# Kernel tuning notes

Hardware: AMD Instinct MI355X
Metric: run time of the kernel (lower is better)

## Reference

```python
import jax, jax.numpy as jnp
import numpy as np

B, E, N, D, L = 16, 1024, 2048, 256, 3


def setup_inputs() -> dict:
    key = jax.random.key(0)
    ks = jax.random.split(key, 8)
    return {
        "evidences_mat": jax.random.normal(ks[0], (B, E, D), jnp.float32),
        "entities_mat": jax.random.normal(ks[1], (B, N, D), jnp.float32),
        "ev_to_ent": jax.random.bernoulli(ks[2], 0.05, (B, E, N)).astype(jnp.float32),
        "ent_to_ev": jax.random.bernoulli(ks[3], 0.05, (B, N, E)).astype(jnp.float32),
        "w_weight": jax.random.normal(ks[4], (L, D, D), jnp.float32) * 0.05,
        "w_bias": jax.random.normal(ks[5], (L, D), jnp.float32) * 0.05,
        "watt_weight": jax.random.normal(ks[6], (L, D, D), jnp.float32) * 0.05,
        "watt_bias": jax.random.normal(ks[7], (L, D), jnp.float32) * 0.05,
    }


def reference(evidences_mat, entities_mat, ev_to_ent, ent_to_ev,
              w_weight, w_bias, watt_weight, watt_bias):
    ev, ent = evidences_mat, entities_mat
    for i in range(L):
        # attention projections (torch Linear: x @ W.T + b)
        pe = jnp.einsum('bed,od->beo', ev, watt_weight[i]) + watt_bias[i]   # [B,E,D]
        pn = jnp.einsum('bnd,od->bno', ent, watt_weight[i]) + watt_bias[i]  # [B,N,D]
        # evidences -> entities messages
        ev_att = jnp.einsum('bed,bnd->ben', pe, pn) * ev_to_ent             # [B,E,N]
        ev_att = jax.nn.softmax(ev_att, axis=1)                              # over E (dim=1)
        msg_ent = jnp.einsum('ben,bed->bnd', ev_att, ev)                     # [B,N,D]
        msg_ent = jnp.einsum('bnd,od->bno', msg_ent, w_weight[i]) + w_bias[i]
        self_ent = jnp.einsum('bnd,od->bno', ent, w_weight[i]) + w_bias[i]
        ent = jax.nn.relu(msg_ent + self_ent)
        # entities -> evidences messages (uses UPDATED entities, as in source)
        ent_att = jnp.einsum('bnd,bed->bne', pn, pe) * ent_to_ev            # [B,N,E]
        ent_att = jax.nn.softmax(ent_att, axis=1)                            # over N (dim=1)
        msg_ev = jnp.einsum('bne,bnd->bed', ent_att, ent)                    # [B,E,D]
        msg_ev = jnp.einsum('bed,od->beo', msg_ev, w_weight[i]) + w_bias[i]
        self_ev = jnp.einsum('bed,od->beo', ev, w_weight[i]) + w_bias[i]
        ev = jax.nn.relu(msg_ev + self_ev)
        # dropout is a no-op (p=0.0 / eval)
    return ent, ev
```

## Files before the change

kernel.cpp:

```cpp
#include <hip/hip_runtime.h>

#define BB 16
#define EE 1024
#define NN 2048
#define DD 256
#define LL 3

typedef _Float16 half8 __attribute__((ext_vector_type(8)));
typedef _Float16 half4 __attribute__((ext_vector_type(4)));
typedef _Float16 half2_t __attribute__((ext_vector_type(2)));
typedef float f32x4 __attribute__((ext_vector_type(4)));

__device__ __forceinline__ void pmerge(float& m, float& s, float m2, float s2) {
    float nm = fmaxf(m, m2);
    s = s * __expf(m - nm) + s2 * __expf(m2 - nm);
    m = nm;
}

__device__ __forceinline__ unsigned pk2(_Float16 a, _Float16 b) {
    union { _Float16 h[2]; unsigned u; } x;
    x.h[0] = a; x.h[1] = b;
    return x.u;
}

__global__ void split_cast(const float* __restrict__ in, _Float16* __restrict__ hi,
                           _Float16* __restrict__ lo, size_t n) {
    size_t stride = (size_t)gridDim.x * blockDim.x * 4;
    for (size_t i = ((size_t)blockIdx.x * blockDim.x + threadIdx.x) * 4; i < n; i += stride) {
        float4 v = *(const float4*)&in[i];
        half4 hh, ll;
        _Float16 h;
        h = (_Float16)v.x; hh[0] = h; ll[0] = (_Float16)(v.x - (float)h);
        h = (_Float16)v.y; hh[1] = h; ll[1] = (_Float16)(v.y - (float)h);
        h = (_Float16)v.z; hh[2] = h; ll[2] = (_Float16)(v.z - (float)h);
        h = (_Float16)v.w; hh[3] = h; ll[3] = (_Float16)(v.w - (float)h);
        *(half4*)&hi[i] = hh;
        *(half4*)&lo[i] = ll;
    }
}

__global__ void cast_u8(const float* __restrict__ in, unsigned char* __restrict__ out, size_t n) {
    size_t stride = (size_t)gridDim.x * blockDim.x * 4;
    for (size_t i = ((size_t)blockIdx.x * blockDim.x + threadIdx.x) * 4; i < n; i += stride) {
        float4 v = *(const float4*)&in[i];
        unsigned int pack = (unsigned int)(unsigned char)v.x |
                            ((unsigned int)(unsigned char)v.y << 8) |
                            ((unsigned int)(unsigned char)v.z << 16) |
                            ((unsigned int)(unsigned char)v.w << 24);
        *(unsigned int*)&out[i] = pack;
    }
}

__global__ void transpose_split(const float* __restrict__ in, _Float16* __restrict__ oh,
                                _Float16* __restrict__ olo, int R, int C) {
    int b = blockIdx.z;
    int c0 = blockIdx.x * 64, r0 = blockIdx.y * 64;
    const float* ib = in + (size_t)b * R * C;
    size_t ob = (size_t)b * R * C;
    __shared__ float tile[64][65];
    int t = threadIdx.x;
    int cl = t & 63, rb = t >> 6;
#pragma unroll
    for (int j = 0; j < 16; j++) {
        int rl = rb + j * 4;
        tile[rl][cl] = ib[(size_t)(r0 + rl) * C + c0 + cl];
    }
    __syncthreads();
    int oc = t >> 2, q = t & 3;
    half8 h0, h1, l0, l1;
#pragma unroll
    for (int i = 0; i < 8; i++) {
        float v = tile[q * 16 + i][oc];
        _Float16 h = (_Float16)v;
        h0[i] = h; l0[i] = (_Float16)(v - (float)h);
    }
#pragma unroll
    for (int i = 0; i < 8; i++) {
        float v = tile[q * 16 + 8 + i][oc];
        _Float16 h = (_Float16)v;
        h1[i] = h; l1[i] = (_Float16)(v - (float)h);
    }
    size_t o = ob + (size_t)(c0 + oc) * R + r0 + q * 16;
    *(half8*)&oh[o] = h0; *(half8*)&oh[o + 8] = h1;
    *(half8*)&olo[o] = l0; *(half8*)&olo[o + 8] = l1;
}

__global__ void transpose_split_perm(const float* __restrict__ in, _Float16* __restrict__ oh,
                                     _Float16* __restrict__ olo, int R, int C) {
    int b = blockIdx.z;
    int c0 = blockIdx.x * 64, r0 = blockIdx.y * 64;
    const float* ib = in + (size_t)b * R * C;
    size_t ob = (size_t)b * R * C;
    __shared__ float tile[64][65];
    int t = threadIdx.x;
    int cl = t & 63, rb = t >> 6;
#pragma unroll
    for (int j = 0; j < 16; j++) {
        int rl = rb + j * 4;
        tile[rl][cl] = ib[(size_t)(r0 + rl) * C + c0 + cl];
    }
    __syncthreads();
    int oc = t >> 2, q = t & 3;
    int g = q >> 1, sub = q & 1;
#pragma unroll
    for (int j = 0; j < 8; j++) {
        int x = sub * 8 + j;
        float v1 = tile[g * 32 + x][oc];
        float v2 = tile[g * 32 + x + 16][oc];
        _Float16 a = (_Float16)v1, b2 = (_Float16)v2;
        _Float16 la = (_Float16)(v1 - (float)a), lb = (_Float16)(v2 - (float)b2);
        size_t o = ob + (size_t)(c0 + oc) * R + r0 + g * 32 + 2 * x;
        half2_t hp; hp[0] = a; hp[1] = b2;
        half2_t lp; lp[0] = la; lp[1] = lb;
        *(half2_t*)&oh[o] = hp;
        *(half2_t*)&olo[o] = lp;
    }
}

__global__ void transpose_u8(const float* __restrict__ in, unsigned char* __restrict__ out,
                             int R, int C) {
    int b = blockIdx.z;
    int c0 = blockIdx.x * 64, r0 = blockIdx.y * 64;
    const float* ib = in + (size_t)b * R * C;
    unsigned char* ob = out + (size_t)b * R * C;
    __shared__ float tile[64][65];
    int t = threadIdx.x;
    int cl = t & 63, rb = t >> 6;
#pragma unroll
    for (int j = 0; j < 16; j++) {
        int rl = rb + j * 4;
        tile[rl][cl] = ib[(size_t)(r0 + rl) * C + c0 + cl];
    }
    __syncthreads();
    int oc = t >> 2, q = t & 3;
    union { unsigned char b[16]; uint4 v; } u;
#pragma unroll
    for (int i = 0; i < 16; i++) u.b[i] = (unsigned char)tile[q * 16 + i][oc];
    size_t o = (size_t)(c0 + oc) * R + r0 + q * 16;
    *(uint4*)&ob[o] = u.v;
}

template <bool A_SPLIT, bool B_SPLIT, bool HAS_BIAS, bool RELU, bool HAS_ADD,
          bool WRITE_F32, bool WRITE_SPLIT, bool B_BATCHED>
__global__ __launch_bounds__(256) void gemm_nt(
    const _Float16* __restrict__ Ah, const _Float16* __restrict__ Al,
    const _Float16* __restrict__ Bh, const _Float16* __restrict__ Bl,
    const float* __restrict__ bias, float bscale,
    const float* __restrict__ addsrc,
    float* __restrict__ Cf, _Float16* __restrict__ Chi, _Float16* __restrict__ Clo,
    int M, int Nn, int K) {
    const int bz = blockIdx.z;
    const int m0 = blockIdx.x * 128, n0 = blockIdx.y * 128;
    const int t = threadIdx.x, lane = t & 63, wid = t >> 6;
    const int wm = wid >> 1, wn = wid & 1;
    const size_t offA = (size_t)bz * M * K;
    const size_t offB = B_BATCHED ? (size_t)bz * Nn * K : (size_t)0;
    const _Float16* Abh = Ah + offA;
    const _Float16* Abl = A_SPLIT ? (Al + offA) : nullptr;
    const _Float16* Bbh = Bh + offB;
    const _Float16* Bbl = B_SPLIT ? (Bl + offB) : nullptr;

    __shared__ _Float16 sAh[128 * 32];
    __shared__ _Float16 sBh[128 * 32];
    __shared__ _Float16 sAl[A_SPLIT ? 128 * 32 : 1];
    __shared__ _Float16 sBl[B_SPLIT ? 128 * 32 : 1];

    f32x4 acc[4][4] = {};
    const int nk = K >> 5;

    auto gA = [&](const _Float16* base, int kt, int q) {
        return *(const uint4*)(base + (size_t)(m0 + (q >> 2)) * K + (kt << 5) + ((q & 3) << 3));
    };
    auto gB = [&](const _Float16* base, int kt, int q) {
        return *(const uint4*)(base + (size_t)(n0 + (q >> 2)) * K + (kt << 5) + ((q & 3) << 3));
    };

    uint4 rah0 = gA(Abh, 0, t), rah1 = gA(Abh, 0, t + 256);
    uint4 rbh0 = gB(Bbh, 0, t), rbh1 = gB(Bbh, 0, t + 256);
    uint4 ral0 = {}, ral1 = {}, rbl0 = {}, rbl1 = {};
    if (A_SPLIT) { ral0 = gA(Abl, 0, t); ral1 = gA(Abl, 0, t + 256); }
    if (B_SPLIT) { rbl0 = gB(Bbl, 0, t); rbl1 = gB(Bbl, 0, t + 256); }

    for (int kt = 0; kt < nk; ++kt) {
        __syncthreads();
        ((uint4*)sAh)[t] = rah0; ((uint4*)sAh)[t + 256] = rah1;
        ((uint4*)sBh)[t] = rbh0; ((uint4*)sBh)[t + 256] = rbh1;
        if (A_SPLIT) { ((uint4*)sAl)[t] = ral0; ((uint4*)sAl)[t + 256] = ral1; }
        if (B_SPLIT) { ((uint4*)sBl)[t] = rbl0; ((uint4*)sBl)[t + 256] = rbl1; }
        __syncthreads();
        if (kt + 1 < nk) {
            rah0 = gA(Abh, kt + 1, t); rah1 = gA(Abh, kt + 1, t + 256);
            rbh0 = gB(Bbh, kt + 1, t); rbh1 = gB(Bbh, kt + 1, t + 256);
            if (A_SPLIT) { ral0 = gA(Abl, kt + 1, t); ral1 = gA(Abl, kt + 1, t + 256); }
            if (B_SPLIT) { rbl0 = gB(Bbl, kt + 1, t); rbl1 = gB(Bbl, kt + 1, t + 256); }
        }
        half8 afh[4], bfh[4], afl[4], bfl[4];
#pragma unroll
        for (int mi = 0; mi < 4; mi++) {
            int off = (wm * 64 + mi * 16 + (lane & 15)) * 32 + ((lane >> 4) << 3);
            afh[mi] = *(const half8*)&sAh[off];
            if (A_SPLIT) afl[mi] = *(const half8*)&sAl[off];
        }
#pragma unroll
        for (int nj = 0; nj < 4; nj++) {
            int off = (wn * 64 + nj * 16 + (lane & 15)) * 32 + ((lane >> 4) << 3);
            bfh[nj] = *(const half8*)&sBh[off];
            if (B_SPLIT) bfl[nj] = *(const half8*)&sBl[off];
        }
#pragma unroll
        for (int mi = 0; mi < 4; mi++)
#pragma unroll
            for (int nj = 0; nj < 4; nj++) {
                acc[mi][nj] = __builtin_amdgcn_mfma_f32_16x16x32_f16(afh[mi], bfh[nj], acc[mi][nj], 0, 0, 0);
                if (B_SPLIT)
                    acc[mi][nj] = __builtin_amdgcn_mfma_f32_16x16x32_f16(afh[mi], bfl[nj], acc[mi][nj], 0, 0, 0);
                if (A_SPLIT)
                    acc[mi][nj] = __builtin_amdgcn_mfma_f32_16x16x32_f16(afl[mi], bfh[nj], acc[mi][nj], 0, 0, 0);
            }
    }

    const int rbase = (lane >> 4) * 4, cc = lane & 15;
#pragma unroll
    for (int mi = 0; mi < 4; mi++) {
#pragma unroll
        for (int nj = 0; nj < 4; nj++) {
            int gn = n0 + wn * 64 + nj * 16 + cc;
            float bv = HAS_BIAS ? bias[gn] * bscale : 0.f;
#pragma unroll
            for (int r = 0; r < 4; r++) {
                int gm = m0 + wm * 64 + mi * 16 + rbase + r;
                float v = acc[mi][nj][r];
                if (HAS_BIAS) v += bv;
                size_t off = ((size_t)bz * M + gm) * Nn + gn;
                if (HAS_ADD) v += addsrc[off];
                if (RELU) v = fmaxf(v, 0.f);
                if (WRITE_F32) Cf[off] = v;
                if (WRITE_SPLIT) {
                    _Float16 h = (_Float16)v;
                    Chi[off] = h;
                    Clo[off] = (_Float16)(v - (float)h);
                }
            }
        }
    }
}

template <bool TRANSA>
__global__ __launch_bounds__(256) void fused_agg(
    const float* __restrict__ S_, const unsigned char* __restrict__ Mk,
    const float2* __restrict__ st, const _Float16* __restrict__ Bh,
    const _Float16* __restrict__ Bl, const float* __restrict__ addsrc,
    _Float16* __restrict__ Xhi, _Float16* __restrict__ Xlo,
    int M, int K) {
    const int bz = blockIdx.z;
    const int m0 = blockIdx.x * 64, n0 = blockIdx.y * 128;
    const int t = threadIdx.x, lane = t & 63, wid = t >> 6;
    const int wm = wid >> 1, wn = wid & 1;
    const float* Sb = S_ + (size_t)bz * EE * NN;
    const unsigned char* Mb = Mk + (size_t)bz * EE * NN;
    const float2* stb = st + (size_t)bz * M;
    const _Float16* Bbh = Bh + (size_t)bz * DD * K;
    const _Float16* Bbl = Bl + (size_t)bz * DD * K;

    __shared__ _Float16 sA[64 * 32];
    __shared__ _Float16 sBh[128 * 32];
    __shared__ _Float16 sBl[128 * 32];

    f32x4 acc[2][4] = {};
    const int nk = K >> 5;

    float stc[4], stem[4];
    if (TRANSA) {
        int ncol = (t & 15) * 4;
#pragma unroll
        for (int i = 0; i < 4; i++) {
            float2 v = stb[m0 + ncol + i];
            stc[i] = v.x; stem[i] = v.y;
        }
    } else {
#pragma unroll
        for (int p = 0; p < 2; p++) {
            float2 v = stb[m0 + (t >> 3) + p * 32];
            stc[p] = v.x; stem[p] = v.y;
        }
    }

    unsigned apack[4];
    uint4 rbh0, rbh1, rbl0, rbl1;

    auto prefA = [&](int kt) {
        if (TRANSA) {
            int r = t >> 4, ncol = (t & 15) * 4, e0 = kt * 32;
            size_t rowoff = (size_t)(e0 + r) * NN + m0 + ncol;
            f32x4 s1 = *(const f32x4*)(Sb + rowoff);
            f32x4 s2 = *(const f32x4*)(Sb + rowoff + (size_t)16 * NN);
            unsigned a1 = *(const unsigned*)(Mb + rowoff);
            unsigned a2 = *(const unsigned*)(Mb + rowoff + (size_t)16 * NN);
#pragma unroll
            for (int i = 0; i < 4; i++) {
                float c = stc[i], em = stem[i];
                float x1 = ((a1 >> (8 * i)) & 255u) ? __expf(s1[i] - c) : em;
                float x2 = ((a2 >> (8 * i)) & 255u) ? __expf(s2[i] - c) : em;
                apack[i] = pk2((_Float16)x1, (_Float16)x2);
            }
        } else {
            int kc = (t & 7) * 4, rb = t >> 3;
#pragma unroll
            for (int p = 0; p < 2; p++) {
                size_t rowoff = (size_t)(m0 + rb + p * 32) * NN + kt * 32 + kc;
                f32x4 s = *(const f32x4*)(Sb + rowoff);
                unsigned a = *(const unsigned*)(Mb + rowoff);
                float c = stc[p], em = stem[p];
                _Float16 h0 = (_Float16)(((a) & 255u) ? __expf(s[0] - c) : em);
                _Float16 h1 = (_Float16)(((a >> 8) & 255u) ? __expf(s[1] - c) : em);
                _Float16 h2 = (_Float16)(((a >> 16) & 255u) ? __expf(s[2] - c) : em);
                _Float16 h3 = (_Float16)(((a >> 24) & 255u) ? __expf(s[3] - c) : em);
                apack[2 * p] = pk2(h0, h1);
                apack[2 * p + 1] = pk2(h2, h3);
            }
        }
    };
    auto prefB = [&](int kt) {
        auto g = [&](const _Float16* base, int q) {
            return *(const uint4*)(base + (size_t)(n0 + (q >> 2)) * K + kt * 32 + (q & 3) * 8);
        };
        rbh0 = g(Bbh, t); rbh1 = g(Bbh, t + 256);
        rbl0 = g(Bbl, t); rbl1 = g(Bbl, t + 256);
    };
    auto storeAB = [&]() {
        if (TRANSA) {
            int r = t >> 4, ncol = (t & 15) * 4;
#pragma unroll
            for (int i = 0; i < 4; i++) {
                int n = ncol + i;
                int cp = (r >> 2) ^ ((n >> 2) & 3);
                ((unsigned*)sA)[n * 16 + cp * 4 + (r & 3)] = apack[i];
            }
        } else {
            int kc = (t & 7) * 4, rb = t >> 3;
#pragma unroll
            for (int p = 0; p < 2; p++) {
                unsigned* dst = (unsigned*)&sA[(rb + p * 32) * 32 + kc];
                dst[0] = apack[2 * p]; dst[1] = apack[2 * p + 1];
            }
        }
        ((uint4*)sBh)[t] = rbh0; ((uint4*)sBh)[t + 256] = rbh1;
        ((uint4*)sBl)[t] = rbl0; ((uint4*)sBl)[t + 256] = rbl1;
    };

    prefA(0); prefB(0);

    for (int kt = 0; kt < nk; ++kt) {
        __syncthreads();
        storeAB();
        __syncthreads();
        if (kt + 1 < nk) { prefA(kt + 1); prefB(kt + 1); }
        half8 af[2], bfh[4], bfl[4];
        const int l4 = lane & 15, h = lane >> 4;
        const int cswz = TRANSA ? (h ^ ((l4 >> 2) & 3)) : h;
#pragma unroll
        for (int mi = 0; mi < 2; mi++)
            af[mi] = *(const half8*)&sA[(wm * 32 + mi * 16 + l4) * 32 + cswz * 8];
#pragma unroll
        for (int nj = 0; nj < 4; nj++) {
            int off = (wn * 64 + nj * 16 + l4) * 32 + h * 8;
            bfh[nj] = *(const half8*)&sBh[off];
            bfl[nj] = *(const half8*)&sBl[off];
        }
#pragma unroll
        for (int mi = 0; mi < 2; mi++)
#pragma unroll
            for (int nj = 0; nj < 4; nj++) {
                acc[mi][nj] = __builtin_amdgcn_mfma_f32_16x16x32_f16(af[mi], bfh[nj], acc[mi][nj], 0, 0, 0);
                acc[mi][nj] = __builtin_amdgcn_mfma_f32_16x16x32_f16(af[mi], bfl[nj], acc[mi][nj], 0, 0, 0);
            }
    }

    const int rbase = (lane >> 4) * 4, cc = lane & 15;
#pragma unroll
    for (int mi = 0; mi < 2; mi++) {
#pragma unroll
        for (int nj = 0; nj < 4; nj++) {
            int gn = n0 + wn * 64 + nj * 16 + cc;
#pragma unroll
            for (int r = 0; r < 4; r++) {
                int gm = m0 + wm * 32 + mi * 16 + rbase + r;
                size_t off = ((size_t)bz * M + gm) * DD + gn;
                float v = acc[mi][nj][r] + addsrc[off];
                _Float16 h = (_Float16)v;
                Xhi[off] = h;
                Xlo[off] = (_Float16)(v - (float)h);
            }
        }
    }
}

__global__ __launch_bounds__(256) void stats(const float* __restrict__ S_,
                                             const unsigned char* __restrict__ m1,
                                             const unsigned char* __restrict__ m2t,
                                             float2* __restrict__ d1p,
                                             float2* __restrict__ d2p) {
    int b = blockIdx.z, e0 = blockIdx.y * 64, n0 = blockIdx.x * 256;
    int t = threadIdx.x, lane = t & 63, w = t >> 6;
    size_t base = ((size_t)b * EE + e0) * NN + n0;

    f32x4 xs[16];
    unsigned int am[16], cm[16];
#pragma unroll
    for (int j = 0; j < 16; j++) {
        size_t off = base + (size_t)(w * 16 + j) * NN + lane * 4;
        float4 s = *(const float4*)(S_ + off);
        xs[j][0] = s.x; xs[j][1] = s.y; xs[j][2] = s.z; xs[j][3] = s.w;
        am[j] = *(const unsigned int*)(m1 + off);
        cm[j] = *(const unsigned int*)(m2t + off);
    }

    float cmx[4], csm[4];
#pragma unroll
    for (int i = 0; i < 4; i++) {
        float mx = ((am[0] >> (8 * i)) & 0xffu) ? xs[0][i] : 0.f;
#pragma unroll
        for (int j = 1; j < 16; j++) {
            float xe = ((am[j] >> (8 * i)) & 0xffu) ? xs[j][i] : 0.f;
            mx = fmaxf(mx, xe);
        }
        float sm = 0.f;
#pragma unroll
        for (int j = 0; j < 16; j++) {
            float xe = ((am[j] >> (8 * i)) & 0xffu) ? xs[j][i] : 0.f;
            sm += __expf(xe - mx);
        }
        cmx[i] = mx; csm[i] = sm;
    }
    __shared__ float rm[4][256], rs[4][256];
#pragma unroll
    for (int i = 0; i < 4; i++) { rm[w][lane * 4 + i] = cmx[i]; rs[w][lane * 4 + i] = csm[i]; }
    __syncthreads();
    {
        float M0 = rm[0][t], S0 = rs[0][t];
#pragma unroll
        for (int ww = 1; ww < 4; ww++) pmerge(M0, S0, rm[ww][t], rs[ww][t]);
        d1p[(size_t)blockIdx.y * (BB * NN) + (size_t)b * NN + n0 + t] = make_float2(M0, S0);
    }

#pragma unroll
    for (int j = 0; j < 16; j++) {
        float x0 = ((cm[j]) & 0xffu) ? xs[j][0] : 0.f;
        float x1 = ((cm[j] >> 8) & 0xffu) ? xs[j][1] : 0.f;
        float x2 = ((cm[j] >> 16) & 0xffu) ? xs[j][2] : 0.f;
        float x3 = ((cm[j] >> 24) & 0xffu) ? xs[j][3] : 0.f;
        float mx = fmaxf(fmaxf(x0, x1), fmaxf(x2, x3));
#pragma unroll
        for (int off = 1; off < 64; off <<= 1) mx = fmaxf(mx, __shfl_xor(mx, off, 64));
        float sm = __expf(x0 - mx) + __expf(x1 - mx) + __expf(x2 - mx) + __expf(x3 - mx);
#pragma unroll
        for (int off = 1; off < 64; off <<= 1) sm += __shfl_xor(sm, off, 64);
        if (lane == 0)
            d2p[(size_t)blockIdx.x * (BB * EE) + (size_t)b * EE + e0 + w * 16 + j] = make_float2(mx, sm);
    }
}

__global__ void reduce_dens(const float2* __restrict__ d1p, const float2* __restrict__ d2p,
                            float2* __restrict__ d1, float2* __restrict__ d2) {
    int i = blockIdx.x * 256 + threadIdx.x;
    if (i < BB * NN) {
        float2 v = d1p[i];
        float m = v.x, s = v.y;
#pragma unroll
        for (int k = 1; k < 16; k++) {
            float2 u = d1p[(size_t)k * (BB * NN) + i];
            pmerge(m, s, u.x, u.y);
        }
        float c = m + __logf(s);
        d1[i] = make_float2(c, __expf(-c));
    } else {
        int j = i - BB * NN;
        if (j < BB * EE) {
            float2 v = d2p[j];
            float m = v.x, s = v.y;
#pragma unroll
            for (int k = 1; k < 8; k++) {
                float2 u = d2p[(size_t)k * (BB * EE) + j];
                pmerge(m, s, u.x, u.y);
            }
            float c = m + __logf(s);
            d2[j] = make_float2(c, __expf(-c));
        }
    }
}

extern "C" void kernel_launch(void* const* d_in, const int* in_sizes, int n_in,
                              void* d_out, int out_size, void* d_ws, size_t ws_size,
                              hipStream_t stream) {
    const float* evid   = (const float*)d_in[0];
    const float* enti   = (const float*)d_in[1];
    const float* ev2ent = (const float*)d_in[2];
    const float* ent2ev = (const float*)d_in[3];
    const float* w_w    = (const float*)d_in[4];
    const float* w_b    = (const float*)d_in[5];
    const float* wa_w   = (const float*)d_in[6];
    const float* wa_b   = (const float*)d_in[7];
    float* out_ent = (float*)d_out;
    float* out_ev  = out_ent + (size_t)BB * NN * DD;

    char* p = (char*)d_ws;
    auto alloc = [&](size_t bytes) {
        char* r = p;
        p += (bytes + 255) & ~(size_t)255;
        return (void*)r;
    };
    const size_t nED = (size_t)BB * EE * DD, nND = (size_t)BB * NN * DD;
    const size_t nEN = (size_t)BB * EE * NN, nW = (size_t)LL * DD * DD;
    _Float16* Whi  = (_Float16*)alloc(nW * 2);
    _Float16* Wlo  = (_Float16*)alloc(nW * 2);
    _Float16* Wahi = (_Float16*)alloc(nW * 2);
    _Float16* Walo = (_Float16*)alloc(nW * 2);
    _Float16* evh  = (_Float16*)alloc(nED * 2);
    _Float16* evl  = (_Float16*)alloc(nED * 2);
    _Float16* enth = (_Float16*)alloc(nND * 2);
    _Float16* entl = (_Float16*)alloc(nND * 2);
    _Float16* evTh = (_Float16*)alloc(nED * 2);
    _Float16* evTl = (_Float16*)alloc(nED * 2);
    _Float16* entTh= (_Float16*)alloc(nND * 2);
    _Float16* entTl= (_Float16*)alloc(nND * 2);
    _Float16* peh  = (_Float16*)alloc(nED * 2);
    _Float16* pel  = (_Float16*)alloc(nED * 2);
    _Float16* pnh  = (_Float16*)alloc(nND * 2);
    _Float16* pnl  = (_Float16*)alloc(nND * 2);
    float*    S    = (float*)alloc(nEN * 4);
    unsigned char* m1  = (unsigned char*)alloc(nEN);
    unsigned char* m2t = (unsigned char*)alloc(nEN);
    float* evS  = (float*)alloc(nED * 4);
    float* entS = (float*)alloc(nND * 4);
    float2* d1p = (float2*)alloc((size_t)16 * BB * NN * 8);
    float2* d2p = (float2*)alloc((size_t)8 * BB * EE * 8);
    float2* d1  = (float2*)alloc((size_t)BB * NN * 8);
    float2* d2  = (float2*)alloc((size_t)BB * EE * 8);
    if ((size_t)(p - (char*)d_ws) > ws_size) return;
    _Float16* Xenth = pnh; _Float16* Xentl = pnl;
    _Float16* Xevh  = peh; _Float16* Xevl  = pel;

    split_cast<<<2048, 256, 0, stream>>>(wa_w, Wahi, Walo, nW);
    split_cast<<<2048, 256, 0, stream>>>(w_w, Whi, Wlo, nW);
    split_cast<<<2048, 256, 0, stream>>>(evid, evh, evl, nED);
    split_cast<<<2048, 256, 0, stream>>>(enti, enth, entl, nND);
    cast_u8<<<2048, 256, 0, stream>>>(ev2ent, m1, nEN);
    transpose_u8<<<dim3(EE / 64, NN / 64, BB), 256, 0, stream>>>(ent2ev, m2t, NN, EE);
    transpose_split_perm<<<dim3(DD / 64, EE / 64, BB), 256, 0, stream>>>(evid, evTh, evTl, EE, DD);
    hipMemcpyAsync(evS, evid, nED * 4, hipMemcpyDeviceToDevice, stream);
    hipMemcpyAsync(entS, enti, nND * 4, hipMemcpyDeviceToDevice, stream);

    for (int i = 0; i < LL; i++) {
        const _Float16* Wih  = Whi + (size_t)i * DD * DD;
        const _Float16* Wil  = Wlo + (size_t)i * DD * DD;
        const _Float16* Waih = Wahi + (size_t)i * DD * DD;
        const _Float16* Wail = Walo + (size_t)i * DD * DD;
        const float* bi  = w_b + i * DD;
        const float* bai = wa_b + i * DD;

        gemm_nt<true, true, true, false, false, false, true, false>
            <<<dim3(EE / 128, DD / 128, BB), 256, 0, stream>>>(
                evh, evl, Waih, Wail, bai, 1.f, nullptr, nullptr, peh, pel, EE, DD, DD);
        gemm_nt<true, true, true, false, false, false, true, false>
            <<<dim3(NN / 128, DD / 128, BB), 256, 0, stream>>>(
                enth, entl, Waih, Wail, bai, 1.f, nullptr, nullptr, pnh, pnl, NN, DD, DD);
        gemm_nt<true, true, false, false, false, true, false, true>
            <<<dim3(EE / 128, NN / 128, BB), 256, 0, stream>>>(
                peh, pel, pnh, pnl, nullptr, 0.f, nullptr, S, nullptr, nullptr, EE, NN, DD);
        stats<<<dim3(NN / 256, EE / 64, BB), 256, 0, stream>>>(S, m1, m2t, d1p, d2p);
        reduce_dens<<<(BB * NN + BB * EE + 255) / 256, 256, 0, stream>>>(d1p, d2p, d1, d2);
        fused_agg<true><<<dim3(NN / 64, 2, BB), 256, 0, stream>>>(
            S, m1, d1, evTh, evTl, entS, Xenth, Xentl, NN, EE);
        float* entDst = (i == LL - 1) ? out_ent : entS;
        gemm_nt<true, true, true, true, false, true, true, false>
            <<<dim3(NN / 128, DD / 128, BB), 256, 0, stream>>>(
                Xenth, Xentl, Wih, Wil, bi, 2.f, nullptr, entDst, enth, entl, NN, DD, DD);
        transpose_split<<<dim3(DD / 64, NN / 64, BB), 256, 0, stream>>>(entDst, entTh, entTl, NN, DD);
        fused_agg<false><<<dim3(EE / 64, 2, BB), 256, 0, stream>>>(
            S, m2t, d2, entTh, entTl, evS, Xevh, Xevl, EE, NN);
        float* evDst = (i == LL - 1) ? out_ev : evS;
        gemm_nt<true, true, true, true, false, true, true, false>
            <<<dim3(EE / 128, DD / 128, BB), 256, 0, stream>>>(
                Xevh, Xevl, Wih, Wil, bi, 2.f, nullptr, evDst, evh, evl, EE, DD, DD);
        if (i < LL - 1)
            transpose_split_perm<<<dim3(DD / 64, EE / 64, BB), 256, 0, stream>>>(evS, evTh, evTl, EE, DD);
    }
}
```

Measured before the change: 1.360 ms.

## Double-buffer raw A-tile loads and defer exp/convert to shared-memory store

Global loads for the masked-softmax A tile now keep raw fp32 scores and mask bytes in registers, two k-tiles ahead, while B stays one tile ahead. The exp and fp16 packing move from the prefetch step into the store step just before writing to shared memory. The loop is unrolled by two to alternate between the two register buffers. This gives global loads more latency slack before use, at the cost of more live registers, which may lower occupancy. The loop assumes nk is even.

```diff
diff --git a/kernel.cpp b/kernel.cpp
--- a/kernel.cpp
+++ b/kernel.cpp
@@ -285,39 +285,26 @@
         }
     }
 
-    unsigned apack[4];
+    struct RawA { f32x4 s1, s2; unsigned a1, a2; };
+    RawA A0, A1;
     uint4 rbh0, rbh1, rbl0, rbl1;
 
-    auto prefA = [&](int kt) {
+    auto prefA_load = [&](RawA& R, int kt) {
         if (TRANSA) {
-            int r = t >> 4, ncol = (t & 15) * 4, e0 = kt * 32;
-            size_t rowoff = (size_t)(e0 + r) * NN + m0 + ncol;
-            f32x4 s1 = *(const f32x4*)(Sb + rowoff);
-            f32x4 s2 = *(const f32x4*)(Sb + rowoff + (size_t)16 * NN);
-            unsigned a1 = *(const unsigned*)(Mb + rowoff);
-            unsigned a2 = *(const unsigned*)(Mb + rowoff + (size_t)16 * NN);
-#pragma unroll
-            for (int i = 0; i < 4; i++) {
-                float c = stc[i], em = stem[i];
-                float x1 = ((a1 >> (8 * i)) & 255u) ? __expf(s1[i] - c) : em;
-                float x2 = ((a2 >> (8 * i)) & 255u) ? __expf(s2[i] - c) : em;
-                apack[i] = pk2((_Float16)x1, (_Float16)x2);
-            }
+            int r = t >> 4, ncol = (t & 15) * 4;
+            size_t rowoff = (size_t)(kt * 32 + r) * NN + m0 + ncol;
+            R.s1 = *(const f32x4*)(Sb + rowoff);
+            R.s2 = *(const f32x4*)(Sb + rowoff + (size_t)16 * NN);
+            R.a1 = *(const unsigned*)(Mb + rowoff);
+            R.a2 = *(const unsigned*)(Mb + rowoff + (size_t)16 * NN);
         } else {
             int kc = (t & 7) * 4, rb = t >> 3;
-#pragma unroll
-            for (int p = 0; p < 2; p++) {
-                size_t rowoff = (size_t)(m0 + rb + p * 32) * NN + kt * 32 + kc;
-                f32x4 s = *(const f32x4*)(Sb + rowoff);
-                unsigned a = *(const unsigned*)(Mb + rowoff);
-                float c = stc[p], em = stem[p];
-                _Float16 h0 = (_Float16)(((a) & 255u) ? __expf(s[0] - c) : em);
-                _Float16 h1 = (_Float16)(((a >> 8) & 255u) ? __expf(s[1] - c) : em);
-                _Float16 h2 = (_Float16)(((a >> 16) & 255u) ? __expf(s[2] - c) : em);
-                _Float16 h3 = (_Float16)(((a >> 24) & 255u) ? __expf(s[3] - c) : em);
-                apack[2 * p] = pk2(h0, h1);
-                apack[2 * p + 1] = pk2(h2, h3);
-            }
+            size_t ro1 = (size_t)(m0 + rb) * NN + kt * 32 + kc;
+            size_t ro2 = (size_t)(m0 + rb + 32) * NN + kt * 32 + kc;
+            R.s1 = *(const f32x4*)(Sb + ro1);
+            R.s2 = *(const f32x4*)(Sb + ro2);
+            R.a1 = *(const unsigned*)(Mb + ro1);
+            R.a2 = *(const unsigned*)(Mb + ro2);
         }
     };
     auto prefB = [&](int kt) {
@@ -327,34 +314,45 @@
         rbh0 = g(Bbh, t); rbh1 = g(Bbh, t + 256);
         rbl0 = g(Bbl, t); rbl1 = g(Bbl, t + 256);
     };
-    auto storeAB = [&]() {
+    auto storeA = [&](RawA& R) {
         if (TRANSA) {
             int r = t >> 4, ncol = (t & 15) * 4;
 #pragma unroll
             for (int i = 0; i < 4; i++) {
+                float c = stc[i], em = stem[i];
+                float x1 = ((R.a1 >> (8 * i)) & 255u) ? __expf(R.s1[i] - c) : em;
+                float x2 = ((R.a2 >> (8 * i)) & 255u) ? __expf(R.s2[i] - c) : em;
                 int n = ncol + i;
                 int cp = (r >> 2) ^ ((n >> 2) & 3);
-                ((unsigned*)sA)[n * 16 + cp * 4 + (r & 3)] = apack[i];
+                ((unsigned*)sA)[n * 16 + cp * 4 + (r & 3)] = pk2((_Float16)x1, (_Float16)x2);
             }
         } else {
             int kc = (t & 7) * 4, rb = t >> 3;
-#pragma unroll
-            for (int p = 0; p < 2; p++) {
-                unsigned* dst = (unsigned*)&sA[(rb + p * 32) * 32 + kc];
-                dst[0] = apack[2 * p]; dst[1] = apack[2 * p + 1];
-            }
-        }
+            {
+                float c = stc[0], em = stem[0];
+                _Float16 h0 = (_Float16)(((R.a1) & 255u) ? __expf(R.s1[0] - c) : em);
+                _Float16 h1 = (_Float16)(((R.a1 >> 8) & 255u) ? __expf(R.s1[1] - c) : em);
+                _Float16 h2 = (_Float16)(((R.a1 >> 16) & 255u) ? __expf(R.s1[2] - c) : em);
+                _Float16 h3 = (_Float16)(((R.a1 >> 24) & 255u) ? __expf(R.s1[3] - c) : em);
+                unsigned* dst = (unsigned*)&sA[rb * 32 + kc];
+                dst[0] = pk2(h0, h1); dst[1] = pk2(h2, h3);
+            }
+            {
+                float c = stc[1], em = stem[1];
+                _Float16 h0 = (_Float16)(((R.a2) & 255u) ? __expf(R.s2[0] - c) : em);
+                _Float16 h1 = (_Float16)(((R.a2 >> 8) & 255u) ? __expf(R.s2[1] - c) : em);
+                _Float16 h2 = (_Float16)(((R.a2 >> 16) & 255u) ? __expf(R.s2[2] - c) : em);
+                _Float16 h3 = (_Float16)(((R.a2 >> 24) & 255u) ? __expf(R.s2[3] - c) : em);
+                unsigned* dst = (unsigned*)&sA[(rb + 32) * 32 + kc];
+                dst[0] = pk2(h0, h1); dst[1] = pk2(h2, h3);
+            }
+        }
+    };
+    auto storeB = [&]() {
         ((uint4*)sBh)[t] = rbh0; ((uint4*)sBh)[t + 256] = rbh1;
         ((uint4*)sBl)[t] = rbl0; ((uint4*)sBl)[t + 256] = rbl1;
     };
-
-    prefA(0); prefB(0);
-
-    for (int kt = 0; kt < nk; ++kt) {
-        __syncthreads();
-        storeAB();
-        __syncthreads();
-        if (kt + 1 < nk) { prefA(kt + 1); prefB(kt + 1); }
+    auto compute = [&]() {
         half8 af[2], bfh[4], bfl[4];
         const int l4 = lane & 15, h = lane >> 4;
         const int cswz = TRANSA ? (h ^ ((l4 >> 2) & 3)) : h;
@@ -374,6 +372,25 @@
                 acc[mi][nj] = __builtin_amdgcn_mfma_f32_16x16x32_f16(af[mi], bfh[nj], acc[mi][nj], 0, 0, 0);
                 acc[mi][nj] = __builtin_amdgcn_mfma_f32_16x16x32_f16(af[mi], bfl[nj], acc[mi][nj], 0, 0, 0);
             }
+    };
+
+    prefA_load(A0, 0);
+    prefA_load(A1, 1);
+    prefB(0);
+
+    for (int kt = 0; kt < nk; kt += 2) {
+        __syncthreads();
+        storeA(A0); storeB();
+        __syncthreads();
+        if (kt + 2 < nk) prefA_load(A0, kt + 2);
+        prefB(kt + 1);
+        compute();
+        __syncthreads();
+        storeA(A1); storeB();
+        __syncthreads();
+        if (kt + 3 < nk) prefA_load(A1, kt + 3);
+        if (kt + 2 < nk) prefB(kt + 2);
+        compute();
     }
 
     const int rbase = (lane >> 4) * 4, cc = lane & 15;
```

New measurement: 1.367 ms. Within noise of the previous version (+0.5%).
